# Kernel tuning notes

Measured on AMD Instinct MI355X. Metric: run time of the kernel, lower is better.

## Reference

```python
import jax, jax.numpy as jnp
import numpy as np

# Config mirrors init_kwargs
H_FULL, W_FULL = 360, 720
SCALE = 4
H_LO, W_LO = H_FULL // SCALE, W_FULL // SCALE  # 90, 180
LMAX = H_LO                  # 90
MMAX = W_LO // 2 + 1         # 91
C = 128                      # embed_dim
NL = 4                       # num_layers
INP_CH, OUT_CH = 2, 2
MLP_HID = int(C * 2.0)
EPS = 1e-5


def rfft2_trunc(x):
    # RealFFT2.forward: ortho rfft2, keep first ceil(LMAX/2) and last floor(LMAX/2) lat modes, first MMAX lon modes
    y = jnp.fft.rfft2(x, norm="ortho")
    lt = (LMAX + 1) // 2
    lb = LMAX - lt
    return jnp.concatenate([y[..., :lt, :MMAX], y[..., y.shape[-2] - lb:, :MMAX]], axis=-2)


def irfft2_pad(y, H, W):
    # InverseRealFFT2: zero-pad truncated modes back to full spectrum, ortho irfft2
    lt = (LMAX + 1) // 2
    lb = LMAX - lt
    full = jnp.zeros(y.shape[:-2] + (H, W // 2 + 1), dtype=y.dtype)
    full = full.at[..., :lt, :MMAX].set(y[..., :lt, :])
    full = full.at[..., H - lb:, :MMAX].set(y[..., lt:, :])
    return jnp.fft.irfft2(full, s=(H, W), norm="ortho")


def inorm(x, w, b):
    # InstanceNorm2d(affine=True): per-sample, per-channel over spatial dims, biased var
    mu = x.mean(axis=(-2, -1), keepdims=True)
    var = x.var(axis=(-2, -1), keepdims=True)
    xn = (x - mu) * jax.lax.rsqrt(var + EPS)
    return xn * w[None, :, None, None] + b[None, :, None, None]


def conv1x1(x, w):  # w: [Cout, Cin], bias=False
    return jnp.einsum('bihw,oi->bohw', x, w)


def gelu(x):
    return jax.nn.gelu(x, approximate=False)


def fno_block(x, n0w, n0b, swr, swi, iw, n1w, n1b, mw1, mw2, out_hw):
    in_hw = x.shape[-2:]
    xn = inorm(x, n0w, n0b)
    # SpectralConv (dhconv): complex per-l channel mixing in truncated spectral space
    Xc = rfft2_trunc(xn)                                   # [B,C,LMAX,MMAX] complex
    scale_res = tuple(in_hw) != tuple(out_hw)
    residual = irfft2_pad(Xc, out_hw[0], out_hw[1]) if scale_res else xn
    w = swr + 1j * swi                                      # [Cin,Cout,LMAX]
    Yc = jnp.einsum('bilm,iol->bolm', Xc, w)
    h = irfft2_pad(Yc, out_hw[0], out_hw[1])
    h = h + conv1x1(residual, iw)                           # inner linear skip
    h = gelu(h)                                             # act_layer0
    h = inorm(h, n1w, n1b)                                  # norm1
    h = conv1x1(gelu(conv1x1(h, mw1)), mw2)                 # MLP (1x1 convs)
    return h + residual                                     # outer identity skip


def setup_inputs() -> dict:
    key = jax.random.key(0)
    ks = jax.random.split(key, 16)
    s = 1.0 / np.sqrt(C)
    inp = {
        "x": jax.random.normal(ks[0], (1, INP_CH, H_FULL, W_FULL), jnp.float32),
        # encoder: inp_chans -> C -> C (encoder_ratio=1)
        "enc_w1": jax.random.normal(ks[1], (C, INP_CH), jnp.float32) * (1.0 / np.sqrt(INP_CH)),
        "enc_w2": jax.random.normal(ks[2], (C, C), jnp.float32) * s,
        # per-layer stacked block params
        "n0w": jnp.ones((NL, C), jnp.float32),
        "n0b": jnp.zeros((NL, C), jnp.float32),
        "swr": jax.random.normal(ks[3], (NL, C, C, LMAX), jnp.float32) * (1.0 / C),
        "swi": jax.random.normal(ks[4], (NL, C, C, LMAX), jnp.float32) * (1.0 / C),
        "iw": jax.random.normal(ks[5], (NL, C, C), jnp.float32) * s,
        "n1w": jnp.ones((NL, C), jnp.float32),
        "n1b": jnp.zeros((NL, C), jnp.float32),
        "mw1": jax.random.normal(ks[6], (NL, MLP_HID, C), jnp.float32) * s,
        "mw2": jax.random.normal(ks[7], (NL, C, MLP_HID), jnp.float32) * (1.0 / np.sqrt(MLP_HID)),
        # decoder: (C + inp_chans) -> C -> out_chans (big_skip concat)
        "dec_w1": jax.random.normal(ks[8], (C, C + INP_CH), jnp.float32) * (1.0 / np.sqrt(C + INP_CH)),
        "dec_w2": jax.random.normal(ks[9], (OUT_CH, C), jnp.float32) * s,
    }
    return inp


def reference(x, enc_w1, enc_w2, n0w, n0b, swr, swi, iw, n1w, n1b, mw1, mw2, dec_w1, dec_w2):
    big_res = x
    h = conv1x1(gelu(conv1x1(x, enc_w1)), enc_w2)           # encoder
    out_shapes = [(H_LO, W_LO)] * (NL - 1) + [(H_FULL, W_FULL)]
    for l in range(NL):
        h = fno_block(h, n0w[l], n0b[l], swr[l], swi[l], iw[l],
                      n1w[l], n1b[l], mw1[l], mw2[l], out_shapes[l])
    h = jnp.concatenate([h, big_res], axis=1)               # big skip
    h = conv1x1(gelu(conv1x1(h, dec_w1)), dec_w2)           # decoder
    return h
```

## Files before the change

kernel.cpp:

```cpp
#include <hip/hip_runtime.h>
#include <hip/hip_bf16.h>
#include <math.h>

typedef __attribute__((ext_vector_type(8))) short short8v;
typedef __attribute__((ext_vector_type(4))) float f32x4;
typedef unsigned short u16;

__device__ __forceinline__ float gelu_f(float x) {
    return 0.5f * x * (1.0f + erff(x * 0.70710678118654752f));
}
__device__ __forceinline__ float bf2f(u16 u) {
    union { unsigned int i; float f; } v; v.i = ((unsigned int)u) << 16; return v.f;
}
__device__ __forceinline__ u16 f2bf(float f) {
    union { float f; unsigned int i; } v; v.f = f;
    unsigned int r = v.i + 0x7FFFu + ((v.i >> 16) & 1u);
    return (u16)(r >> 16);
}
__device__ __forceinline__ short8v negbf(short8v a) {
    uint4 u = *(uint4*)&a;
    u.x ^= 0x80008000u; u.y ^= 0x80008000u; u.z ^= 0x80008000u; u.w ^= 0x80008000u;
    return *(short8v*)&u;
}

__device__ __forceinline__ uint4 load8(const u16* p) { return *(const uint4*)p; }
__device__ __forceinline__ uint4 load8(const float* p) {
    float4 a = *(const float4*)p;
    float4 b = *(const float4*)(p + 4);
    union { uint4 u; u16 e[8]; } r;
    r.e[0] = f2bf(a.x); r.e[1] = f2bf(a.y); r.e[2] = f2bf(a.z); r.e[3] = f2bf(a.w);
    r.e[4] = f2bf(b.x); r.e[5] = f2bf(b.y); r.e[6] = f2bf(b.z); r.e[7] = f2bf(b.w);
    return r.u;
}
__device__ __forceinline__ float rdD(const u16* p) { return bf2f(*p); }
__device__ __forceinline__ float rdD(const float* p) { return *p; }
__device__ __forceinline__ void stO(u16* p, float v) { *p = f2bf(v); }
__device__ __forceinline__ void stO(float* p, float v) { *p = v; }

template<int BMODE, class TA, class TB, class TD, class TO>
__global__ __launch_bounds__(256) void gemm_t(
    const TA* __restrict__ A1, const TB* __restrict__ B1,
    const TA* __restrict__ A2, const TB* __restrict__ B2,
    const TD* __restrict__ D, TO* __restrict__ O,
    int M, int N, int Kp, int neg2, int act,
    long long sAb, long long sAm,
    long long sBb, long long sBr,
    long long sDb, long long sDm,
    long long sOb, long long sOm)
{
    __shared__ __align__(16) u16 As[64 * 32];
    __shared__ __align__(16) u16 Bs[BMODE ? 32 * 68 : 64 * 32];
    const int tid = threadIdx.x;
    const long long b = blockIdx.z;
    const int bm0 = blockIdx.y * 64;
    const int bn0 = blockIdx.x * 64;
    const int lane = tid & 63;
    const int wave = tid >> 6;
    const int wr = (wave >> 1) * 32;
    const int wc = (wave & 1) * 32;
    const int fr = lane & 15;
    const int fg = lane >> 4;
    const int arow = tid >> 2, achk = tid & 3;

    f32x4 acc[2][2];
#pragma unroll
    for (int i = 0; i < 2; ++i)
#pragma unroll
        for (int j = 0; j < 2; ++j) acc[i][j] = (f32x4){0.f, 0.f, 0.f, 0.f};

    const int nph = A2 ? 2 : 1;
    for (int ph = 0; ph < nph; ++ph) {
        const TA* Ap = (ph ? A2 : A1) + b * sAb;
        const TB* Bp = (ph ? B2 : B1) + b * sBb;
        const unsigned int sgn = (ph && neg2) ? 0x80008000u : 0u;
        for (int k0 = 0; k0 < Kp; k0 += 32) {
            uint4 av = load8(Ap + (long long)(bm0 + arow) * sAm + k0 + achk * 8);
            av.x ^= sgn; av.y ^= sgn; av.z ^= sgn; av.w ^= sgn;
            uint4 bv;
            if (BMODE == 0) {
                bv = load8(Bp + (long long)(bn0 + arow) * sBr + k0 + achk * 8);
            } else {
                const int bk = tid >> 3, bnc = tid & 7;
                bv = load8(Bp + (long long)(k0 + bk) * sBr + bn0 + bnc * 8);
            }
            __syncthreads();
            *(uint4*)(&As[arow * 32 + ((achk ^ ((arow >> 1) & 3)) * 8)]) = av;
            if (BMODE == 0) {
                *(uint4*)(&Bs[arow * 32 + ((achk ^ ((arow >> 1) & 3)) * 8)]) = bv;
            } else {
                const int bk = tid >> 3, bnc = tid & 7;
                *(uint2*)(&Bs[bk * 68 + bnc * 8]) = make_uint2(bv.x, bv.y);
                *(uint2*)(&Bs[bk * 68 + bnc * 8 + 4]) = make_uint2(bv.z, bv.w);
            }
            __syncthreads();
            short8v afrag[2], bfrag[2];
#pragma unroll
            for (int i = 0; i < 2; ++i) {
                int r = wr + i * 16 + fr;
                afrag[i] = *(const short8v*)(&As[r * 32 + ((fg ^ ((r >> 1) & 3)) * 8)]);
            }
            if (BMODE == 0) {
#pragma unroll
                for (int j = 0; j < 2; ++j) {
                    int r = wc + j * 16 + fr;
                    bfrag[j] = *(const short8v*)(&Bs[r * 32 + ((fg ^ ((r >> 1) & 3)) * 8)]);
                }
            } else {
#pragma unroll
                for (int j = 0; j < 2; ++j) {
                    int col = wc + j * 16 + fr;
                    short8v v;
#pragma unroll
                    for (int e = 0; e < 8; ++e) v[e] = (short)Bs[(fg * 8 + e) * 68 + col];
                    bfrag[j] = v;
                }
            }
#pragma unroll
            for (int i = 0; i < 2; ++i)
#pragma unroll
                for (int j = 0; j < 2; ++j)
                    acc[i][j] = __builtin_amdgcn_mfma_f32_16x16x32_bf16(afrag[i], bfrag[j], acc[i][j], 0, 0, 0);
        }
    }
#pragma unroll
    for (int i = 0; i < 2; ++i) {
#pragma unroll
        for (int j = 0; j < 2; ++j) {
            int col = bn0 + wc + j * 16 + fr;
            if (col >= N) continue;
#pragma unroll
            for (int r = 0; r < 4; ++r) {
                int row = bm0 + wr + i * 16 + fg * 4 + r;
                if (row >= M) continue;
                float v = acc[i][j][r];
                if (D) v += rdD(D + b * sDb + (long long)row * sDm + col);
                if (act) v = gelu_f(v);
                stO(O + b * sOb + (long long)row * sOm + col, v);
            }
        }
    }
}

template<class TA, class TB, class TD, class TO>
__global__ __launch_bounds__(256) void gemm_ts(
    const TA* __restrict__ A, const TB* __restrict__ B,
    const TD* __restrict__ D, TO* __restrict__ O,
    int M, int N, int Kp, int act,
    long long sAm, long long sBr,
    long long sDm, long long sOm)
{
    __shared__ __align__(16) u16 As[64 * 32];
    __shared__ __align__(16) u16 Bs[64 * 32];
    const int tid = threadIdx.x;
    int lid = blockIdx.x + (int)gridDim.x * blockIdx.y;
    int total = (int)(gridDim.x * gridDim.y);
    int nx, ny;
    if ((lid & ~15) + 16 <= total) {
        nx = (lid >> 3) & 1;
        ny = ((lid >> 4) << 3) + (lid & 7);
    } else {
        nx = lid & 1;
        ny = lid >> 1;
    }
    const int bm0 = ny * 64;
    const int bn0 = nx * 64;
    const int lane = tid & 63;
    const int wave = tid >> 6;
    const int wr = (wave >> 1) * 32;
    const int wc = (wave & 1) * 32;
    const int fr = lane & 15;
    const int fg = lane >> 4;
    const int arow = tid >> 2, achk = tid & 3;
    const int aswz = (achk ^ ((arow >> 1) & 3)) * 8;

    f32x4 acc[2][2];
#pragma unroll
    for (int i = 0; i < 2; ++i)
#pragma unroll
        for (int j = 0; j < 2; ++j) acc[i][j] = (f32x4){0.f, 0.f, 0.f, 0.f};

    for (int k0 = 0; k0 < Kp; k0 += 32) {
        uint4 av = load8(A + (long long)(bm0 + arow) * sAm + k0 + achk * 8);
        uint4 bv = load8(B + (long long)(bn0 + arow) * sBr + k0 + achk * 8);
        __syncthreads();
        *(uint4*)(&As[arow * 32 + aswz]) = av;
        *(uint4*)(&Bs[arow * 32 + aswz]) = bv;
        __syncthreads();
        short8v afrag[2], bfrag[2];
#pragma unroll
        for (int i = 0; i < 2; ++i) {
            int r = wr + i * 16 + fr;
            afrag[i] = *(const short8v*)(&As[r * 32 + ((fg ^ ((r >> 1) & 3)) * 8)]);
        }
#pragma unroll
        for (int j = 0; j < 2; ++j) {
            int r = wc + j * 16 + fr;
            bfrag[j] = *(const short8v*)(&Bs[r * 32 + ((fg ^ ((r >> 1) & 3)) * 8)]);
        }
#pragma unroll
        for (int i = 0; i < 2; ++i)
#pragma unroll
            for (int j = 0; j < 2; ++j)
                acc[i][j] = __builtin_amdgcn_mfma_f32_16x16x32_bf16(afrag[i], bfrag[j], acc[i][j], 0, 0, 0);
    }
#pragma unroll
    for (int i = 0; i < 2; ++i) {
#pragma unroll
        for (int j = 0; j < 2; ++j) {
            int col = bn0 + wc + j * 16 + fr;
            if (col >= N) continue;
#pragma unroll
            for (int r = 0; r < 4; ++r) {
                int row = bm0 + wr + i * 16 + fg * 4 + r;
                if (row >= M) continue;
                float v = acc[i][j][r];
                if (D) v += rdD(D + (long long)row * sDm + col);
                if (act) v = gelu_f(v);
                stO(O + (long long)row * sOm + col, v);
            }
        }
    }
}

template<int BMODE, int MODE, class TA, class TB, class TO>
__global__ __launch_bounds__(256) void gemm_t2(
    const TA* __restrict__ A1, const TA* __restrict__ A2,
    const TB* __restrict__ B1, const TB* __restrict__ B2,
    TO* __restrict__ O1, TO* __restrict__ O2,
    int M, int N, int Kp, int s2neg,
    long long sAb, long long sAm,
    long long sBb, long long sBr,
    long long sOb, long long sOm)
{
    __shared__ __align__(16) u16 As1[64 * 32], As2[64 * 32];
    __shared__ __align__(16) u16 Bs1[BMODE ? 32 * 68 : 64 * 32];
    __shared__ __align__(16) u16 Bs2[(MODE == 1) ? 16 : (BMODE ? 32 * 68 : 64 * 32)];
    const int tid = threadIdx.x;
    const long long b = blockIdx.z;
    const int bm0 = blockIdx.y * 64;
    const int bn0 = blockIdx.x * 64;
    const int lane = tid & 63;
    const int wave = tid >> 6;
    const int wr = (wave >> 1) * 32;
    const int wc = (wave & 1) * 32;
    const int fr = lane & 15;
    const int fg = lane >> 4;
    const int arow = tid >> 2, achk = tid & 3;
    const int aswz = (achk ^ ((arow >> 1) & 3)) * 8;

    f32x4 acc1[2][2], acc2[2][2];
#pragma unroll
    for (int i = 0; i < 2; ++i)
#pragma unroll
        for (int j = 0; j < 2; ++j) {
            acc1[i][j] = (f32x4){0.f, 0.f, 0.f, 0.f};
            acc2[i][j] = (f32x4){0.f, 0.f, 0.f, 0.f};
        }

    const TA* A1b = A1 + b * sAb;
    const TA* A2b = A2 + b * sAb;
    const TB* B1b = B1 + b * sBb;
    const TB* B2b = (MODE == 0) ? B2 + b * sBb : B1;

    for (int k0 = 0; k0 < Kp; k0 += 32) {
        long long aoff = (long long)(bm0 + arow) * sAm + k0 + achk * 8;
        uint4 av1 = load8(A1b + aoff);
        uint4 av2 = load8(A2b + aoff);
        uint4 bv1, bv2;
        if (BMODE == 0) {
            long long boff = (long long)(bn0 + arow) * sBr + k0 + achk * 8;
            bv1 = load8(B1b + boff);
            if (MODE == 0) bv2 = load8(B2b + boff);
        } else {
            const int bk = tid >> 3, bnc = tid & 7;
            long long boff = (long long)(k0 + bk) * sBr + bn0 + bnc * 8;
            bv1 = load8(B1b + boff);
            if (MODE == 0) bv2 = load8(B2b + boff);
        }
        __syncthreads();
        *(uint4*)(&As1[arow * 32 + aswz]) = av1;
        *(uint4*)(&As2[arow * 32 + aswz]) = av2;
        if (BMODE == 0) {
            *(uint4*)(&Bs1[arow * 32 + aswz]) = bv1;
            if (MODE == 0) *(uint4*)(&Bs2[arow * 32 + aswz]) = bv2;
        } else {
            const int bk = tid >> 3, bnc = tid & 7;
            *(uint2*)(&Bs1[bk * 68 + bnc * 8]) = make_uint2(bv1.x, bv1.y);
            *(uint2*)(&Bs1[bk * 68 + bnc * 8 + 4]) = make_uint2(bv1.z, bv1.w);
            if (MODE == 0) {
                *(uint2*)(&Bs2[bk * 68 + bnc * 8]) = make_uint2(bv2.x, bv2.y);
                *(uint2*)(&Bs2[bk * 68 + bnc * 8 + 4]) = make_uint2(bv2.z, bv2.w);
            }
        }
        __syncthreads();
        short8v a1f[2], a2f[2], b1f[2], b2f[2];
#pragma unroll
        for (int i = 0; i < 2; ++i) {
            int r = wr + i * 16 + fr;
            int o = r * 32 + ((fg ^ ((r >> 1) & 3)) * 8);
            a1f[i] = *(const short8v*)(&As1[o]);
            a2f[i] = *(const short8v*)(&As2[o]);
        }
        if (BMODE == 0) {
#pragma unroll
            for (int j = 0; j < 2; ++j) {
                int r = wc + j * 16 + fr;
                int o = r * 32 + ((fg ^ ((r >> 1) & 3)) * 8);
                b1f[j] = *(const short8v*)(&Bs1[o]);
                if (MODE == 0) b2f[j] = *(const short8v*)(&Bs2[o]);
            }
        } else {
#pragma unroll
            for (int j = 0; j < 2; ++j) {
                int col = wc + j * 16 + fr;
                short8v v1, v2;
#pragma unroll
                for (int e = 0; e < 8; ++e) {
                    v1[e] = (short)Bs1[(fg * 8 + e) * 68 + col];
                    if (MODE == 0) v2[e] = (short)Bs2[(fg * 8 + e) * 68 + col];
                }
                b1f[j] = v1;
                if (MODE == 0) b2f[j] = v2;
            }
        }
        if (MODE == 1) {
#pragma unroll
            for (int i = 0; i < 2; ++i)
#pragma unroll
                for (int j = 0; j < 2; ++j) {
                    acc1[i][j] = __builtin_amdgcn_mfma_f32_16x16x32_bf16(a1f[i], b1f[j], acc1[i][j], 0, 0, 0);
                    acc2[i][j] = __builtin_amdgcn_mfma_f32_16x16x32_bf16(a2f[i], b1f[j], acc2[i][j], 0, 0, 0);
                }
        } else {
            short8v a2p[2], a2m[2];
#pragma unroll
            for (int i = 0; i < 2; ++i) {
                a2p[i] = s2neg ? negbf(a2f[i]) : a2f[i];
                a2m[i] = s2neg ? a2f[i] : negbf(a2f[i]);
            }
#pragma unroll
            for (int i = 0; i < 2; ++i)
#pragma unroll
                for (int j = 0; j < 2; ++j) {
                    acc1[i][j] = __builtin_amdgcn_mfma_f32_16x16x32_bf16(a1f[i], b1f[j], acc1[i][j], 0, 0, 0);
                    acc1[i][j] = __builtin_amdgcn_mfma_f32_16x16x32_bf16(a2p[i], b2f[j], acc1[i][j], 0, 0, 0);
                    acc2[i][j] = __builtin_amdgcn_mfma_f32_16x16x32_bf16(a1f[i], b2f[j], acc2[i][j], 0, 0, 0);
                    acc2[i][j] = __builtin_amdgcn_mfma_f32_16x16x32_bf16(a2m[i], b1f[j], acc2[i][j], 0, 0, 0);
                }
        }
    }
#pragma unroll
    for (int i = 0; i < 2; ++i) {
#pragma unroll
        for (int j = 0; j < 2; ++j) {
            int col = bn0 + wc + j * 16 + fr;
            if (col >= N) continue;
#pragma unroll
            for (int r = 0; r < 4; ++r) {
                int row = bm0 + wr + i * 16 + fg * 4 + r;
                if (row >= M) continue;
                long long oi = b * sOb + (long long)row * sOm + col;
                stO(O1 + oi, acc1[i][j][r]);
                stO(O2 + oi, acc2[i][j][r]);
            }
        }
    }
}

__global__ void gen_fwdW_T(u16* Cm, u16* Sm, int RP, int KP, int W, int MM) {
    int idx = blockIdx.x * blockDim.x + threadIdx.x;
    if (idx >= RP * KP) return;
    int m = idx / KP, w = idx % KP;
    float cv = 0.f, sv = 0.f;
    if (m < MM && w < W) {
        int t = (m * w) % W;
        float arg = 2.0f * (float)t / (float)W;
        float s = 1.0f / sqrtf((float)W);
        cv = cospif(arg) * s; sv = -sinpif(arg) * s;
    }
    Cm[idx] = f2bf(cv); Sm[idx] = f2bf(sv);
}
__global__ void gen_fwdH(u16* Cm, u16* Sm, int RP, int KP, int H) {
    int idx = blockIdx.x * blockDim.x + threadIdx.x;
    if (idx >= RP * KP) return;
    int l = idx / KP, h = idx % KP;
    float cv = 0.f, sv = 0.f;
    if (l < 90 && h < H) {
        int ll = (l < 45) ? l : l + H - 90;
        int t = (ll * h) % H;
        float arg = 2.0f * (float)t / (float)H;
        float s = 1.0f / sqrtf((float)H);
        cv = cospif(arg) * s; sv = sinpif(arg) * s;
    }
    Cm[idx] = f2bf(cv); Sm[idx] = f2bf(sv);
}
__global__ void gen_invH(u16* Cm, u16* Sm, int RP, int KP, int H) {
    int idx = blockIdx.x * blockDim.x + threadIdx.x;
    if (idx >= RP * KP) return;
    int y = idx / KP, l = idx % KP;
    float cv = 0.f, sv = 0.f;
    if (y < H && l < 90) {
        int ll = (l < 45) ? l : l + H - 90;
        int t = (ll * y) % H;
        float arg = 2.0f * (float)t / (float)H;
        float s = 1.0f / sqrtf((float)H);
        cv = cospif(arg) * s; sv = sinpif(arg) * s;
    }
    Cm[idx] = f2bf(cv); Sm[idx] = f2bf(sv);
}
__global__ void gen_invW_T(u16* Cm, u16* Sm, int RP, int KP, int W, int MM) {
    int idx = blockIdx.x * blockDim.x + threadIdx.x;
    if (idx >= RP * KP) return;
    int w = idx / KP, m = idx % KP;
    float cv = 0.f, sv = 0.f;
    if (w < W && m < MM) {
        int t = (m * w) % W;
        float arg = 2.0f * (float)t / (float)W;
        bool nyq = (2 * m == W);
        float wt = (m == 0 || nyq) ? 1.0f : 2.0f;
        float s = wt / sqrtf((float)W);
        cv = cospif(arg) * s;
        sv = nyq ? 0.f : sinpif(arg) * s;
    }
    Cm[idx] = f2bf(cv); Sm[idx] = f2bf(sv);
}

__global__ void w2bf(const float* __restrict__ in, u16* __restrict__ out, int R, int K, int rs) {
    int idx = blockIdx.x * blockDim.x + threadIdx.x;
    if (idx >= R * K) return;
    int r = idx / K, c = idx % K;
    out[idx] = f2bf(in[(long long)r * rs + c]);
}
__global__ void transp_sw(const float* __restrict__ in, u16* __restrict__ out) {
    __shared__ float t[32][33];
    int l0 = blockIdx.x * 32, ci0 = blockIdx.y * 32, co = blockIdx.z;
    int tx = threadIdx.x, ty = threadIdx.y;
#pragma unroll
    for (int rr = 0; rr < 4; ++rr) {
        int ci = ci0 + ty + rr * 8;
        int l = l0 + tx;
        t[ty + rr * 8][tx] = (l < 90) ? in[((long long)ci * 128 + co) * 90 + l] : 0.f;
    }
    __syncthreads();
#pragma unroll
    for (int rr = 0; rr < 4; ++rr) {
        int l = l0 + ty + rr * 8;
        int ci = ci0 + tx;
        if (l < 90) out[((long long)l * 128 + co) * 128 + ci] = f2bf(t[tx][ty + rr * 8]);
    }
}

__global__ __launch_bounds__(256) void stats_cl_bf(const u16* __restrict__ x, long long P,
                                                   float2* __restrict__ part, int nch) {
    int chunk = blockIdx.x;
    int c = threadIdx.x & 127;
    int h = threadIdx.x >> 7;
    long long beg = P * chunk / nch, end = P * (chunk + 1) / nch;
    float s = 0.f, q = 0.f;
    long long p = beg + h;
    for (; p + 14 < end; p += 16) {
        float v[8];
#pragma unroll
        for (int u = 0; u < 8; ++u) v[u] = bf2f(x[(p + 2 * u) * 128 + c]);
#pragma unroll
        for (int u = 0; u < 8; ++u) { s += v[u]; q += v[u] * v[u]; }
    }
    for (; p < end; p += 2) {
        float v = bf2f(x[p * 128 + c]);
        s += v; q += v * v;
    }
    __shared__ float rs[256], rq[256];
    rs[threadIdx.x] = s; rq[threadIdx.x] = q;
    __syncthreads();
    if (threadIdx.x < 128)
        part[(long long)c * nch + chunk] = make_float2(rs[c] + rs[c + 128], rq[c] + rq[c + 128]);
}
__global__ __launch_bounds__(256) void stats_cl_f32(const float* __restrict__ x, long long P,
                                                    float2* __restrict__ part, int nch) {
    int chunk = blockIdx.x;
    long long beg = P * chunk / nch, end = P * (chunk + 1) / nch;
    int c32 = threadIdx.x & 31;
    int pr  = threadIdx.x >> 5;
    float s[4], q[4];
#pragma unroll
    for (int k = 0; k < 4; ++k) { s[k] = 0.f; q[k] = 0.f; }
    for (long long p = beg + pr; p < end; p += 8) {
        float4 v = *(const float4*)(x + p * 128 + c32 * 4);
        float e[4] = {v.x, v.y, v.z, v.w};
#pragma unroll
        for (int k = 0; k < 4; ++k) { s[k] += e[k]; q[k] += e[k] * e[k]; }
    }
#pragma unroll
    for (int k = 0; k < 4; ++k) {
        s[k] += __shfl_xor(s[k], 32); q[k] += __shfl_xor(q[k], 32);
    }
    __shared__ float2 lds[4][128];
    int wv = threadIdx.x >> 6, lane = threadIdx.x & 63;
    if (lane < 32) {
#pragma unroll
        for (int k = 0; k < 4; ++k) lds[wv][lane * 4 + k] = make_float2(s[k], q[k]);
    }
    __syncthreads();
    if (threadIdx.x < 128) {
        float2 a = lds[0][threadIdx.x], b2 = lds[1][threadIdx.x];
        float2 c2 = lds[2][threadIdx.x], d2 = lds[3][threadIdx.x];
        part[(long long)threadIdx.x * nch + chunk] =
            make_float2(a.x + b2.x + c2.x + d2.x, a.y + b2.y + c2.y + d2.y);
    }
}
__global__ void stats_fin(const float2* __restrict__ part, int nch, float Pf,
                          const float* __restrict__ w, const float* __restrict__ b,
                          float2* __restrict__ st) {
    int c = threadIdx.x;
    float s = 0.f, q = 0.f;
    for (int i = 0; i < nch; ++i) { float2 p = part[(long long)c * nch + i]; s += p.x; q += p.y; }
    float mu = s / Pf;
    float var = q / Pf - mu * mu;
    float inv = rsqrtf(var + 1e-5f);
    float sc = w[c] * inv;
    st[c] = make_float2(sc, b[c] - mu * sc);
}
__global__ __launch_bounds__(256) void norm_apply_bf(const u16* __restrict__ src, u16* __restrict__ dst,
                                                     long long n8, const float2* __restrict__ st) {
    long long i = (long long)blockIdx.x * 256 + threadIdx.x;
    if (i >= n8) return;
    int c0 = (int)((i * 8) & 127);
    uint4 v = *(const uint4*)(src + i * 8);
    union { uint4 u; u16 e[8]; } in, out;
    in.u = v;
#pragma unroll
    for (int k = 0; k < 8; ++k) {
        float2 s = st[c0 + k];
        out.e[k] = f2bf(bf2f(in.e[k]) * s.x + s.y);
    }
    *(uint4*)(dst + i * 8) = out.u;
}
__global__ __launch_bounds__(256) void norm_apply_f32(const float4* __restrict__ src, float4* __restrict__ dst,
                                                      long long n4, const float2* __restrict__ st) {
    long long i = (long long)blockIdx.x * 256 + threadIdx.x;
    if (i >= n4) return;
    int c0 = (int)((i * 4) & 127);
    float4 v = src[i];
    float2 s0 = st[c0], s1 = st[c0 + 1], s2 = st[c0 + 2], s3 = st[c0 + 3];
    v.x = v.x * s0.x + s0.y;
    v.y = v.y * s1.x + s1.y;
    v.z = v.z * s2.x + s2.y;
    v.w = v.w * s3.x + s3.y;
    dst[i] = v;
}

__global__ __launch_bounds__(256) void enc_front(const float* __restrict__ x, const float* __restrict__ w1,
                                                 u16* __restrict__ out, long long P) {
    long long idx = (long long)blockIdx.x * 256 + threadIdx.x;
    if (idx >= P * 16) return;
    long long p = idx >> 4;
    int c0 = (int)(idx & 15) * 8;
    float x0 = x[p], x1 = x[P + p];
    union { uint4 u; u16 e[8]; } o;
#pragma unroll
    for (int k = 0; k < 8; ++k) {
        int c = c0 + k;
        o.e[k] = f2bf(gelu_f(w1[c * 2] * x0 + w1[c * 2 + 1] * x1));
    }
    *(uint4*)(out + p * 128 + c0) = o.u;
}
__global__ __launch_bounds__(256) void dec_mid(u16* __restrict__ s, const float* __restrict__ dw1,
                                               const float* __restrict__ x, long long P) {
    long long idx = (long long)blockIdx.x * 256 + threadIdx.x;
    if (idx >= P * 16) return;
    long long p = idx >> 4;
    int c0 = (int)(idx & 15) * 8;
    float x0 = x[p], x1 = x[P + p];
    union { uint4 u; u16 e[8]; } io;
    io.u = *(const uint4*)(s + p * 128 + c0);
#pragma unroll
    for (int k = 0; k < 8; ++k) {
        int c = c0 + k;
        io.e[k] = f2bf(gelu_f(bf2f(io.e[k]) + dw1[c * 130 + 128] * x0 + dw1[c * 130 + 129] * x1));
    }
    *(uint4*)(s + p * 128 + c0) = io.u;
}
__global__ __launch_bounds__(256) void dec_back(const u16* __restrict__ d1, const float* __restrict__ w2,
                                                float* __restrict__ out, long long P) {
    __shared__ float w2s[256];
    w2s[threadIdx.x] = w2[threadIdx.x];
    __syncthreads();
    int lane = threadIdx.x & 63;
    long long pix = (long long)blockIdx.x * 4 + (threadIdx.x >> 6);
    unsigned int pr = *(const unsigned int*)(d1 + pix * 128 + lane * 2);
    float b0 = bf2f((u16)(pr & 0xFFFF)), b1 = bf2f((u16)(pr >> 16));
    float s0 = b0 * w2s[lane * 2] + b1 * w2s[lane * 2 + 1];
    float s1 = b0 * w2s[128 + lane * 2] + b1 * w2s[128 + lane * 2 + 1];
#pragma unroll
    for (int off = 1; off < 64; off <<= 1) {
        s0 += __shfl_xor(s0, off);
        s1 += __shfl_xor(s1, off);
    }
    if (lane == 0) { out[pix] = s0; out[P + pix] = s1; }
}

__global__ void zero_out(float* p, long long n) {
    long long i = (long long)blockIdx.x * 256 + threadIdx.x;
    if (i < n) p[i] = 0.f;
}

extern "C" void kernel_launch(void* const* d_in, const int* in_sizes, int n_in,
                              void* d_out, int out_size, void* d_ws, size_t ws_size,
                              hipStream_t stream)
{
    const int HF = 360, WF = 720, HL = 90, WL = 180, C = 128, MM = 91;
    const long long PF = (long long)HF * WF;
    const long long PL = (long long)HL * WL;
    (void)in_sizes; (void)n_in;

    const float* x      = (const float*)d_in[0];
    const float* enc_w1 = (const float*)d_in[1];
    const float* enc_w2 = (const float*)d_in[2];
    const float* n0w    = (const float*)d_in[3];
    const float* n0b    = (const float*)d_in[4];
    const float* swr    = (const float*)d_in[5];
    const float* swi    = (const float*)d_in[6];
    const float* iw     = (const float*)d_in[7];
    const float* n1w    = (const float*)d_in[8];
    const float* n1b    = (const float*)d_in[9];
    const float* mw1    = (const float*)d_in[10];
    const float* mw2    = (const float*)d_in[11];
    const float* dec_w1 = (const float*)d_in[12];
    const float* dec_w2 = (const float*)d_in[13];
    float* outp = (float*)d_out;

    u16* ws = (u16*)d_ws;
    long long off = 0;
    auto alloc = [&](long long n) { u16* p = ws + off; off += (n + 31) & ~31LL; return p; };
    auto allocF = [&](long long n) { return (float*)alloc(2 * n); };

    u16*   FULL = alloc(PF * C);
    u16*   RES  = alloc(PF * C);
    u16*   S1r  = alloc(96LL * 384 * 128);
    u16*   S1i  = alloc(96LL * 384 * 128);
    float* Xr   = allocF(96LL * 96 * 128);
    float* Xi   = allocF(96LL * 96 * 128);
    float* Yr   = allocF(96LL * 96 * 128);
    float* Yi   = allocF(96LL * 96 * 128);
    u16*   G1r  = alloc(360LL * 96 * 128);
    u16*   G1i  = alloc(360LL * 96 * 128);
    u16*   G3r  = alloc(360LL * 96 * 128);
    u16*   G3i  = alloc(360LL * 96 * 128);
    float* Rlo  = allocF(PL * C);
    float* L0   = allocF(PL * C);
    u16*   HID  = alloc(43200LL * 256);
    u16*   WtR  = alloc(90LL * 128 * 128);
    u16*   WtI  = alloc(90LL * 128 * 128);
    u16* encw2b = alloc(128 * 128);
    u16* iwb    = alloc(128 * 128);
    u16* m1b    = alloc(256 * 128);
    u16* m2b    = alloc(128 * 256);
    u16* dw1b   = alloc(128 * 128);
    u16* CwTc_h = alloc(128 * 736); u16* CwTs_h = alloc(128 * 736);
    u16* CwTc_l = alloc(128 * 192); u16* CwTs_l = alloc(128 * 192);
    u16* Chc_h  = alloc(128 * 384); u16* Chs_h  = alloc(128 * 384);
    u16* Chc_l  = alloc(128 * 96);  u16* Chs_l  = alloc(128 * 96);
    u16* C2c_h  = alloc(384 * 96);  u16* C2s_h  = alloc(384 * 96);
    u16* C2c_l  = alloc(128 * 96);  u16* C2s_l  = alloc(128 * 96);
    u16* CwIc_h = alloc(768 * 96);  u16* CwIs_h = alloc(768 * 96);
    u16* CwIc_l = alloc(192 * 96);  u16* CwIs_l = alloc(192 * 96);
    float2* PART = (float2*)alloc(128 * 256 * 4);
    float2* STb  = (float2*)alloc(128 * 4);
    alloc(64 * 1024);

    if ((size_t)(off * 2) > ws_size) {
        zero_out<<<(int)((out_size + 255) / 256), 256, 0, stream>>>(outp, out_size);
        return;
    }

    auto grid3 = [](int M, int N, int batch) {
        return dim3((unsigned)((N + 63) / 64), (unsigned)((M + 63) / 64), (unsigned)batch);
    };
    auto inormB = [&](const u16* src, u16* dst, long long P, int nch,
                      const float* w, const float* b) {
        stats_cl_bf<<<nch, 256, 0, stream>>>(src, P, PART, nch);
        stats_fin<<<1, 128, 0, stream>>>(PART, nch, (float)P, w, b, STb);
        long long n8 = P * 128 / 8;
        norm_apply_bf<<<(int)((n8 + 255) / 256), 256, 0, stream>>>(src, dst, n8, STb);
    };
    auto inormF = [&](const float* src, float* dst, long long P, int nch,
                      const float* w, const float* b) {
        stats_cl_f32<<<nch, 256, 0, stream>>>(src, P, PART, nch);
        stats_fin<<<1, 128, 0, stream>>>(PART, nch, (float)P, w, b, STb);
        long long n4 = P * 128 / 4;
        norm_apply_f32<<<(int)((n4 + 255) / 256), 256, 0, stream>>>(
            (const float4*)src, (float4*)dst, n4, STb);
    };

    const u16* nullU = nullptr;
    const float* nullF = nullptr;

    {
        int n;
        n = 128 * 736; gen_fwdW_T<<<(n + 255) / 256, 256, 0, stream>>>(CwTc_h, CwTs_h, 128, 736, 720, MM);
        n = 128 * 192; gen_fwdW_T<<<(n + 255) / 256, 256, 0, stream>>>(CwTc_l, CwTs_l, 128, 192, 180, MM);
        n = 128 * 384; gen_fwdH<<<(n + 255) / 256, 256, 0, stream>>>(Chc_h, Chs_h, 128, 384, 360);
        n = 128 * 96;  gen_fwdH<<<(n + 255) / 256, 256, 0, stream>>>(Chc_l, Chs_l, 128, 96, 90);
        n = 384 * 96;  gen_invH<<<(n + 255) / 256, 256, 0, stream>>>(C2c_h, C2s_h, 384, 96, 360);
        n = 128 * 96;  gen_invH<<<(n + 255) / 256, 256, 0, stream>>>(C2c_l, C2s_l, 128, 96, 90);
        n = 768 * 96;  gen_invW_T<<<(n + 255) / 256, 256, 0, stream>>>(CwIc_h, CwIs_h, 768, 96, 720, MM);
        n = 192 * 96;  gen_invW_T<<<(n + 255) / 256, 256, 0, stream>>>(CwIc_l, CwIs_l, 192, 96, 180, MM);
        n = 128 * 128; w2bf<<<(n + 255) / 256, 256, 0, stream>>>(enc_w2, encw2b, 128, 128, 128);
        n = 128 * 128; w2bf<<<(n + 255) / 256, 256, 0, stream>>>(dec_w1, dw1b, 128, 128, 130);
    }

    enc_front<<<(int)((PF * 16 + 255) / 256), 256, 0, stream>>>(x, enc_w1, RES, PF);
    gemm_ts<u16, u16, u16, u16><<<grid3((int)PF, 128, 1), 256, 0, stream>>>(
        RES, encw2b, nullU, FULL, (int)PF, 128, 128, 0, 128, 128, 0, 128);

    const long long s96 = 96LL * 128;

    for (int l = 0; l < 4; ++l) {
        const bool inHi = (l == 0), outHi = (l == 3);
        const int Hin = inHi ? HF : HL, Win = inHi ? WF : WL;
        const int Hout = outHi ? HF : HL, Wout = outHi ? WF : WL;
        const long long Pout = (long long)Hout * Wout;
        const int hdim = inHi ? 384 : 96;
        const int Wp = inHi ? 736 : 192;
        const int hp = inHi ? 384 : 96;
        const u16* CwTc = inHi ? CwTc_h : CwTc_l;  const u16* CwTs = inHi ? CwTs_h : CwTs_l;
        const u16* Chc  = inHi ? Chc_h  : Chc_l;   const u16* Chs  = inHi ? Chs_h  : Chs_l;
        const u16* C2c  = outHi ? C2c_h : C2c_l;   const u16* C2s  = outHi ? C2s_h : C2s_l;
        const u16* CwIc = outHi ? CwIc_h : CwIc_l; const u16* CwIs = outHi ? CwIs_h : CwIs_l;

        {
            dim3 gt(3, 4, 128); dim3 bt(32, 8);
            transp_sw<<<gt, bt, 0, stream>>>(swr + (long long)l * C * C * 90, WtR);
            transp_sw<<<gt, bt, 0, stream>>>(swi + (long long)l * C * C * 90, WtI);
            int n = 128 * 128; w2bf<<<(n + 255) / 256, 256, 0, stream>>>(iw + (long long)l * C * C, iwb, 128, 128, 128);
            n = 256 * 128; w2bf<<<(n + 255) / 256, 256, 0, stream>>>(mw1 + (long long)l * 256 * C, m1b, 256, 128, 128);
            n = 128 * 256; w2bf<<<(n + 255) / 256, 256, 0, stream>>>(mw2 + (long long)l * C * 256, m2b, 128, 256, 256);
        }

        if (inHi) {
            inormB(FULL, RES, PF, 256, n0w + l * C, n0b + l * C);
            gemm_t2<1, 1, u16, u16, u16><<<grid3(96, 128, Hin), 256, 0, stream>>>(
                CwTc, CwTs, RES, nullU, S1r, S1i, 96, 128, Wp, 0,
                0, Wp, (long long)Win * 128, 128, 128, (long long)hdim * 128);
        } else {
            inormF(Rlo, L0, PL, 128, n0w + l * C, n0b + l * C);
            gemm_t2<1, 1, u16, float, u16><<<grid3(96, 128, Hin), 256, 0, stream>>>(
                CwTc, CwTs, L0, nullF, S1r, S1i, 96, 128, Wp, 0,
                0, Wp, (long long)Win * 128, 128, 128, (long long)hdim * 128);
        }

        gemm_t2<1, 0, u16, u16, float><<<grid3(96, 128, 96), 256, 0, stream>>>(
            Chc, Chs, S1r, S1i, Xr, Xi, 96, 128, hp, 0,
            0, hp, (long long)hdim * 128, 128, 128, s96);

        if (inHi || outHi) {
            gemm_t2<1, 0, u16, float, u16><<<grid3(Hout, 128, 96), 256, 0, stream>>>(
                C2c, C2s, Xr, Xi, G3r, G3i, Hout, 128, 96, 1,
                0, 96, 128, s96, 128, s96);
        }

        gemm_t2<0, 0, float, u16, float><<<grid3(96, 128, 90), 256, 0, stream>>>(
            Xr, Xi, WtR, WtI, Yr, Yi, 96, 128, 128, 1,
            s96, 128, 128LL * 128, 128, 128, s96);

        gemm_t2<1, 0, u16, float, u16><<<grid3(Hout, 128, 96), 256, 0, stream>>>(
            C2c, C2s, Yr, Yi, G1r, G1i, Hout, 128, 96, 1,
            0, 96, s96, 128, 128, s96);

        if (!outHi) {
            gemm_t<1, u16, u16, u16, float><<<grid3(Wout, 128, Hout), 256, 0, stream>>>(
                CwIc, G1r, CwIs, G1i, nullU, Rlo, Wout, 128, 96, 1, 0,
                0, 96, s96, 128, 0, 0, (long long)Wout * 128, 128);
            if (inHi)
                gemm_t<1, u16, u16, u16, float><<<grid3(Wout, 128, Hout), 256, 0, stream>>>(
                    CwIc, G3r, CwIs, G3i, nullU, L0, Wout, 128, 96, 1, 0,
                    0, 96, s96, 128, 0, 0, (long long)Wout * 128, 128);
            gemm_t<0, float, u16, float, float><<<grid3((int)Pout, 128, 1), 256, 0, stream>>>(
                L0, iwb, nullF, nullU, Rlo, Rlo, (int)Pout, 128, 128, 0, 1,
                0, 128, 0, 128, 0, 128, 0, 128);
            inormF(Rlo, Rlo, Pout, 128, n1w + l * C, n1b + l * C);
            gemm_t<0, float, u16, u16, u16><<<grid3((int)Pout, 256, 1), 256, 0, stream>>>(
                Rlo, m1b, nullF, nullU, nullU, HID, (int)Pout, 256, 128, 0, 1,
                0, 128, 0, 128, 0, 0, 0, 256);
            gemm_t<0, u16, u16, float, float><<<grid3((int)Pout, 128, 1), 256, 0, stream>>>(
                HID, m2b, nullU, nullU, L0, Rlo, (int)Pout, 128, 256, 0, 0,
                0, 256, 0, 256, 0, 128, 0, 128);
        } else {
            gemm_t<1, u16, u16, u16, u16><<<grid3(Wout, 128, Hout), 256, 0, stream>>>(
                CwIc, G1r, CwIs, G1i, nullU, FULL, Wout, 128, 96, 1, 0,
                0, 96, s96, 128, 0, 0, (long long)Wout * 128, 128);
            gemm_t<1, u16, u16, u16, u16><<<grid3(Wout, 128, Hout), 256, 0, stream>>>(
                CwIc, G3r, CwIs, G3i, nullU, RES, Wout, 128, 96, 1, 0,
                0, 96, s96, 128, 0, 0, (long long)Wout * 128, 128);
            gemm_ts<u16, u16, u16, u16><<<grid3((int)Pout, 128, 1), 256, 0, stream>>>(
                RES, iwb, FULL, FULL, (int)Pout, 128, 128, 1, 128, 128, 128, 128);
            inormB(FULL, FULL, Pout, 256, n1w + l * C, n1b + l * C);
            const int nchunk = 6;
            const long long chM = Pout / nchunk;
            for (int ch = 0; ch < nchunk; ++ch) {
                long long o2 = ch * chM * 128;
                gemm_t<0, u16, u16, u16, u16><<<grid3((int)chM, 256, 1), 256, 0, stream>>>(
                    FULL + o2, m1b, nullU, nullU, nullU, HID, (int)chM, 256, 128, 0, 1,
                    0, 128, 0, 128, 0, 0, 0, 256);
                gemm_ts<u16, u16, u16, u16><<<grid3((int)chM, 128, 1), 256, 0, stream>>>(
                    HID, m2b, RES + o2, FULL + o2, (int)chM, 128, 256, 0, 256, 256, 128, 128);
            }
        }
    }

    gemm_ts<u16, u16, u16, u16><<<grid3((int)PF, 128, 1), 256, 0, stream>>>(
        FULL, dw1b, nullU, RES, (int)PF, 128, 128, 0, 128, 128, 0, 128);
    dec_mid<<<(int)((PF * 16 + 255) / 256), 256, 0, stream>>>(RES, dec_w1, x, PF);
    dec_back<<<(int)(PF / 4), 256, 0, stream>>>(RES, dec_w2, outp, PF);
}
```

Before: 1.285 ms.

## Fuse MLP two GEMMs into one kernel with LDS hidden tile; fuse decoder tail

Adds a gemm_mlp kernel that computes the hidden layer for a 64-row tile, applies GELU, keeps the 64x256 bf16 hidden tile in shared memory, then runs the second GEMM with the residual add. This removes the HID global round-trip and the chunked launch loop for the full-resolution layer. Separately, dec_mid and dec_back are merged so the decoder's skip term and GELU are applied on the fly, avoiding one pass over the full-resolution buffer. The price is that weights are read straight from global memory rather than staged in LDS, the kernel uses about 48KB of LDS (which may lower occupancy), and the A-tile load has no row bound check.

```diff
diff --git a/kernel.cpp b/kernel.cpp
--- a/kernel.cpp
+++ b/kernel.cpp
@@ -217,6 +217,117 @@
                 if (D) v += rdD(D + (long long)row * sDm + col);
                 if (act) v = gelu_f(v);
                 stO(O + (long long)row * sOm + col, v);
+            }
+        }
+    }
+}
+
+template<class TA, class TD, class TO>
+__global__ __launch_bounds__(256) void gemm_mlp(
+    const TA* __restrict__ A, const u16* __restrict__ W1, const u16* __restrict__ W2,
+    const TD* __restrict__ D, TO* __restrict__ O,
+    int M, long long sAm, long long sDm, long long sOm)
+{
+    __shared__ __align__(16) u16 As4[4][64 * 32];
+    __shared__ __align__(16) u16 Hs[8][64 * 32];
+    const int tid = threadIdx.x;
+    const int bm0 = blockIdx.x * 64;
+    const int lane = tid & 63;
+    const int wave = tid >> 6;
+    const int wr = (wave >> 1) * 32;
+    const int wc = (wave & 1) * 32;
+    const int fr = lane & 15;
+    const int fg = lane >> 4;
+    const int arow = tid >> 2, achk = tid & 3;
+    const int aswz = (achk ^ ((arow >> 1) & 3)) * 8;
+
+#pragma unroll
+    for (int kt = 0; kt < 4; ++kt) {
+        uint4 av = load8(A + (long long)(bm0 + arow) * sAm + kt * 32 + achk * 8);
+        *(uint4*)(&As4[kt][arow * 32 + aswz]) = av;
+    }
+    __syncthreads();
+
+#pragma unroll
+    for (int nb = 0; nb < 4; ++nb) {
+        f32x4 acc[2][2];
+#pragma unroll
+        for (int i = 0; i < 2; ++i)
+#pragma unroll
+            for (int j = 0; j < 2; ++j) acc[i][j] = (f32x4){0.f, 0.f, 0.f, 0.f};
+#pragma unroll
+        for (int kt = 0; kt < 4; ++kt) {
+            short8v af[2], bf[2];
+#pragma unroll
+            for (int i = 0; i < 2; ++i) {
+                int r = wr + i * 16 + fr;
+                af[i] = *(const short8v*)(&As4[kt][r * 32 + ((fg ^ ((r >> 1) & 3)) * 8)]);
+            }
+#pragma unroll
+            for (int j = 0; j < 2; ++j) {
+                int col = wc + nb * 64 + j * 16 + fr;
+                bf[j] = *(const short8v*)(W1 + (long long)col * 128 + kt * 32 + fg * 8);
+            }
+#pragma unroll
+            for (int i = 0; i < 2; ++i)
+#pragma unroll
+                for (int j = 0; j < 2; ++j)
+                    acc[i][j] = __builtin_amdgcn_mfma_f32_16x16x32_bf16(af[i], bf[j], acc[i][j], 0, 0, 0);
+        }
+#pragma unroll
+        for (int i = 0; i < 2; ++i)
+#pragma unroll
+            for (int j = 0; j < 2; ++j) {
+                int col = wc + nb * 64 + j * 16 + fr;
+                int kt2 = col >> 5, kc = (col >> 3) & 3, ke = col & 7;
+#pragma unroll
+                for (int r = 0; r < 4; ++r) {
+                    int row = wr + i * 16 + fg * 4 + r;
+                    Hs[kt2][row * 32 + ((kc ^ ((row >> 1) & 3)) * 8) + ke] = f2bf(gelu_f(acc[i][j][r]));
+                }
+            }
+    }
+    __syncthreads();
+
+#pragma unroll
+    for (int nb2 = 0; nb2 < 2; ++nb2) {
+        f32x4 acc2[2][2];
+#pragma unroll
+        for (int i = 0; i < 2; ++i)
+#pragma unroll
+            for (int j = 0; j < 2; ++j) acc2[i][j] = (f32x4){0.f, 0.f, 0.f, 0.f};
+#pragma unroll
+        for (int kt = 0; kt < 8; ++kt) {
+            short8v af[2], bf[2];
+#pragma unroll
+            for (int i = 0; i < 2; ++i) {
+                int r = wr + i * 16 + fr;
+                af[i] = *(const short8v*)(&Hs[kt][r * 32 + ((fg ^ ((r >> 1) & 3)) * 8)]);
+            }
+#pragma unroll
+            for (int j = 0; j < 2; ++j) {
+                int col = nb2 * 64 + wc + j * 16 + fr;
+                bf[j] = *(const short8v*)(W2 + (long long)col * 256 + kt * 32 + fg * 8);
+            }
+#pragma unroll
+            for (int i = 0; i < 2; ++i)
+#pragma unroll
+                for (int j = 0; j < 2; ++j)
+                    acc2[i][j] = __builtin_amdgcn_mfma_f32_16x16x32_bf16(af[i], bf[j], acc2[i][j], 0, 0, 0);
+        }
+#pragma unroll
+        for (int i = 0; i < 2; ++i) {
+#pragma unroll
+            for (int j = 0; j < 2; ++j) {
+                int col = nb2 * 64 + wc + j * 16 + fr;
+#pragma unroll
+                for (int r = 0; r < 4; ++r) {
+                    int row = bm0 + wr + i * 16 + fg * 4 + r;
+                    if (row >= M) continue;
+                    float v = acc2[i][j][r];
+                    if (D) v += rdD(D + (long long)row * sDm + col);
+                    stO(O + (long long)row * sOm + col, v);
+                }
             }
         }
     }
@@ -564,31 +675,23 @@
     }
     *(uint4*)(out + p * 128 + c0) = o.u;
 }
-__global__ __launch_bounds__(256) void dec_mid(u16* __restrict__ s, const float* __restrict__ dw1,
-                                               const float* __restrict__ x, long long P) {
-    long long idx = (long long)blockIdx.x * 256 + threadIdx.x;
-    if (idx >= P * 16) return;
-    long long p = idx >> 4;
-    int c0 = (int)(idx & 15) * 8;
-    float x0 = x[p], x1 = x[P + p];
-    union { uint4 u; u16 e[8]; } io;
-    io.u = *(const uint4*)(s + p * 128 + c0);
-#pragma unroll
-    for (int k = 0; k < 8; ++k) {
-        int c = c0 + k;
-        io.e[k] = f2bf(gelu_f(bf2f(io.e[k]) + dw1[c * 130 + 128] * x0 + dw1[c * 130 + 129] * x1));
-    }
-    *(uint4*)(s + p * 128 + c0) = io.u;
-}
-__global__ __launch_bounds__(256) void dec_back(const u16* __restrict__ d1, const float* __restrict__ w2,
+__global__ __launch_bounds__(256) void dec_fuse(const u16* __restrict__ d1, const float* __restrict__ dw1,
+                                                const float* __restrict__ x, const float* __restrict__ w2,
                                                 float* __restrict__ out, long long P) {
     __shared__ float w2s[256];
+    __shared__ float dxs[256];
     w2s[threadIdx.x] = w2[threadIdx.x];
+    {
+        int c = threadIdx.x >> 1, h = threadIdx.x & 1;
+        dxs[threadIdx.x] = dw1[c * 130 + 128 + h];
+    }
     __syncthreads();
     int lane = threadIdx.x & 63;
     long long pix = (long long)blockIdx.x * 4 + (threadIdx.x >> 6);
+    float x0 = x[pix], x1 = x[P + pix];
     unsigned int pr = *(const unsigned int*)(d1 + pix * 128 + lane * 2);
-    float b0 = bf2f((u16)(pr & 0xFFFF)), b1 = bf2f((u16)(pr >> 16));
+    float b0 = bf2f(f2bf(gelu_f(bf2f((u16)(pr & 0xFFFF)) + dxs[4 * lane]     * x0 + dxs[4 * lane + 1] * x1)));
+    float b1 = bf2f(f2bf(gelu_f(bf2f((u16)(pr >> 16))    + dxs[4 * lane + 2] * x0 + dxs[4 * lane + 3] * x1)));
     float s0 = b0 * w2s[lane * 2] + b1 * w2s[lane * 2 + 1];
     float s1 = b0 * w2s[128 + lane * 2] + b1 * w2s[128 + lane * 2 + 1];
 #pragma unroll
@@ -648,7 +751,6 @@
     u16*   G3i  = alloc(360LL * 96 * 128);
     float* Rlo  = allocF(PL * C);
     float* L0   = allocF(PL * C);
-    u16*   HID  = alloc(43200LL * 256);
     u16*   WtR  = alloc(90LL * 128 * 128);
     u16*   WtI  = alloc(90LL * 128 * 128);
     u16* encw2b = alloc(128 * 128);
@@ -779,12 +881,8 @@
                 L0, iwb, nullF, nullU, Rlo, Rlo, (int)Pout, 128, 128, 0, 1,
                 0, 128, 0, 128, 0, 128, 0, 128);
             inormF(Rlo, Rlo, Pout, 128, n1w + l * C, n1b + l * C);
-            gemm_t<0, float, u16, u16, u16><<<grid3((int)Pout, 256, 1), 256, 0, stream>>>(
-                Rlo, m1b, nullF, nullU, nullU, HID, (int)Pout, 256, 128, 0, 1,
-                0, 128, 0, 128, 0, 0, 0, 256);
-            gemm_t<0, u16, u16, float, float><<<grid3((int)Pout, 128, 1), 256, 0, stream>>>(
-                HID, m2b, nullU, nullU, L0, Rlo, (int)Pout, 128, 256, 0, 0,
-                0, 256, 0, 256, 0, 128, 0, 128);
+            gemm_mlp<float, float, float><<<dim3((unsigned)((Pout + 63) / 64)), 256, 0, stream>>>(
+                Rlo, m1b, m2b, L0, Rlo, (int)Pout, 128, 128, 128);
         } else {
             gemm_t<1, u16, u16, u16, u16><<<grid3(Wout, 128, Hout), 256, 0, stream>>>(
                 CwIc, G1r, CwIs, G1i, nullU, FULL, Wout, 128, 96, 1, 0,
@@ -795,21 +893,12 @@
             gemm_ts<u16, u16, u16, u16><<<grid3((int)Pout, 128, 1), 256, 0, stream>>>(
                 RES, iwb, FULL, FULL, (int)Pout, 128, 128, 1, 128, 128, 128, 128);
             inormB(FULL, FULL, Pout, 256, n1w + l * C, n1b + l * C);
-            const int nchunk = 6;
-            const long long chM = Pout / nchunk;
-            for (int ch = 0; ch < nchunk; ++ch) {
-                long long o2 = ch * chM * 128;
-                gemm_t<0, u16, u16, u16, u16><<<grid3((int)chM, 256, 1), 256, 0, stream>>>(
-                    FULL + o2, m1b, nullU, nullU, nullU, HID, (int)chM, 256, 128, 0, 1,
-                    0, 128, 0, 128, 0, 0, 0, 256);
-                gemm_ts<u16, u16, u16, u16><<<grid3((int)chM, 128, 1), 256, 0, stream>>>(
-                    HID, m2b, RES + o2, FULL + o2, (int)chM, 128, 256, 0, 256, 256, 128, 128);
-            }
+            gemm_mlp<u16, u16, u16><<<dim3((unsigned)((Pout + 63) / 64)), 256, 0, stream>>>(
+                FULL, m1b, m2b, RES, FULL, (int)Pout, 128, 128, 128);
         }
     }
 
     gemm_ts<u16, u16, u16, u16><<<grid3((int)PF, 128, 1), 256, 0, stream>>>(
         FULL, dw1b, nullU, RES, (int)PF, 128, 128, 0, 128, 128, 0, 128);
-    dec_mid<<<(int)((PF * 16 + 255) / 256), 256, 0, stream>>>(RES, dec_w1, x, PF);
-    dec_back<<<(int)(PF / 4), 256, 0, stream>>>(RES, dec_w2, outp, PF);
-}
+    dec_fuse<<<(int)(PF / 4), 256, 0, stream>>>(RES, dec_w1, x, dec_w2, outp, PF);
+}
```

Result: faster. 1.242 ms (median of 3 runs) (-3.4%).

## Fuse MLP GEMMs through LDS and merge decoder mid/back kernels

Applied to the files above, without the earlier changes.

Adds a gemm_mlp kernel that computes the first MLP GEMM with GELU for a 64-row tile, stages the bf16 hidden activations in per-wave LDS, and feeds them straight into the second GEMM plus residual add. This removes the HID intermediate buffer's global write and read and the chunked two-kernel launch loop, for both the low-res and full-res layers. Weight fragments are read directly from global/L2 by every wave instead of being tiled through shared memory, which may add L2 traffic. The decoder's bias/GELU step is folded into the final 2-channel projection kernel, saving one full-resolution pass over the activation tensor.

```diff
diff --git a/kernel.cpp b/kernel.cpp
--- a/kernel.cpp
+++ b/kernel.cpp
@@ -218,6 +218,68 @@
                 if (act) v = gelu_f(v);
                 stO(O + (long long)row * sOm + col, v);
             }
+        }
+    }
+}
+
+template<class TA, class TD, class TO>
+__global__ __launch_bounds__(256) void gemm_mlp(
+    const TA* __restrict__ A, const u16* __restrict__ W1, const u16* __restrict__ W2,
+    const TD* __restrict__ D, TO* __restrict__ O,
+    int M, long long sAm, long long sDm, long long sOm)
+{
+    __shared__ __align__(16) unsigned int Hw[4][16 * 132];
+    const int tid = threadIdx.x;
+    const int bm0 = blockIdx.x * 64;
+    const int lane = tid & 63;
+    const int wave = tid >> 6;
+    const int p = lane & 15;
+    const int g = lane >> 4;
+    const int R0 = bm0 + wave * 16;
+
+    short8v xfrag[4];
+#pragma unroll
+    for (int kt = 0; kt < 4; ++kt) {
+        uint4 v = load8(A + (long long)(R0 + p) * sAm + kt * 32 + g * 8);
+        xfrag[kt] = *(short8v*)&v;
+    }
+
+    unsigned int* Hrow = &Hw[wave][p * 132];
+
+#pragma unroll
+    for (int h = 0; h < 16; ++h) {
+        f32x4 acc = (f32x4){0.f, 0.f, 0.f, 0.f};
+#pragma unroll
+        for (int kt = 0; kt < 4; ++kt) {
+            short8v wf = *(const short8v*)(W1 + (long long)(h * 16 + p) * 128 + kt * 32 + g * 8);
+            acc = __builtin_amdgcn_mfma_f32_16x16x32_bf16(wf, xfrag[kt], acc, 0, 0, 0);
+        }
+        unsigned int lo = (unsigned int)f2bf(gelu_f(acc[0])) | ((unsigned int)f2bf(gelu_f(acc[1])) << 16);
+        unsigned int hi = (unsigned int)f2bf(gelu_f(acc[2])) | ((unsigned int)f2bf(gelu_f(acc[3])) << 16);
+        *(uint2*)(Hrow + 8 * h + 2 * g) = make_uint2(lo, hi);
+    }
+
+    short8v hfrag[8];
+#pragma unroll
+    for (int c = 0; c < 8; ++c)
+        hfrag[c] = *(const short8v*)(Hrow + 16 * c + 4 * g);
+
+#pragma unroll
+    for (int o = 0; o < 8; ++o) {
+        f32x4 acc = (f32x4){0.f, 0.f, 0.f, 0.f};
+#pragma unroll
+        for (int c = 0; c < 8; ++c) {
+            short8v wf = *(const short8v*)(W2 + (long long)(o * 16 + p) * 256 + c * 32 + g * 8);
+            acc = __builtin_amdgcn_mfma_f32_16x16x32_bf16(hfrag[c], wf, acc, 0, 0, 0);
+        }
+        int col = o * 16 + p;
+#pragma unroll
+        for (int r = 0; r < 4; ++r) {
+            int row = R0 + g * 4 + r;
+            if (row >= M) continue;
+            float v = acc[r];
+            if (D) v += rdD(D + (long long)row * sDm + col);
+            stO(O + (long long)row * sOm + col, v);
         }
     }
 }
@@ -564,31 +626,23 @@
     }
     *(uint4*)(out + p * 128 + c0) = o.u;
 }
-__global__ __launch_bounds__(256) void dec_mid(u16* __restrict__ s, const float* __restrict__ dw1,
-                                               const float* __restrict__ x, long long P) {
-    long long idx = (long long)blockIdx.x * 256 + threadIdx.x;
-    if (idx >= P * 16) return;
-    long long p = idx >> 4;
-    int c0 = (int)(idx & 15) * 8;
-    float x0 = x[p], x1 = x[P + p];
-    union { uint4 u; u16 e[8]; } io;
-    io.u = *(const uint4*)(s + p * 128 + c0);
-#pragma unroll
-    for (int k = 0; k < 8; ++k) {
-        int c = c0 + k;
-        io.e[k] = f2bf(gelu_f(bf2f(io.e[k]) + dw1[c * 130 + 128] * x0 + dw1[c * 130 + 129] * x1));
-    }
-    *(uint4*)(s + p * 128 + c0) = io.u;
-}
-__global__ __launch_bounds__(256) void dec_back(const u16* __restrict__ d1, const float* __restrict__ w2,
+__global__ __launch_bounds__(256) void dec_fuse(const u16* __restrict__ d1, const float* __restrict__ dw1,
+                                                const float* __restrict__ x, const float* __restrict__ w2,
                                                 float* __restrict__ out, long long P) {
     __shared__ float w2s[256];
+    __shared__ float dxsT[256];
     w2s[threadIdx.x] = w2[threadIdx.x];
+    {
+        int k = threadIdx.x >> 6, ln = threadIdx.x & 63;
+        dxsT[threadIdx.x] = dw1[(2 * ln + (k >> 1)) * 130 + 128 + (k & 1)];
+    }
     __syncthreads();
     int lane = threadIdx.x & 63;
     long long pix = (long long)blockIdx.x * 4 + (threadIdx.x >> 6);
+    float x0 = x[pix], x1 = x[P + pix];
     unsigned int pr = *(const unsigned int*)(d1 + pix * 128 + lane * 2);
-    float b0 = bf2f((u16)(pr & 0xFFFF)), b1 = bf2f((u16)(pr >> 16));
+    float b0 = bf2f(f2bf(gelu_f(bf2f((u16)(pr & 0xFFFF)) + dxsT[lane]       * x0 + dxsT[64 + lane]  * x1)));
+    float b1 = bf2f(f2bf(gelu_f(bf2f((u16)(pr >> 16))    + dxsT[128 + lane] * x0 + dxsT[192 + lane] * x1)));
     float s0 = b0 * w2s[lane * 2] + b1 * w2s[lane * 2 + 1];
     float s1 = b0 * w2s[128 + lane * 2] + b1 * w2s[128 + lane * 2 + 1];
 #pragma unroll
@@ -648,7 +702,6 @@
     u16*   G3i  = alloc(360LL * 96 * 128);
     float* Rlo  = allocF(PL * C);
     float* L0   = allocF(PL * C);
-    u16*   HID  = alloc(43200LL * 256);
     u16*   WtR  = alloc(90LL * 128 * 128);
     u16*   WtI  = alloc(90LL * 128 * 128);
     u16* encw2b = alloc(128 * 128);
@@ -779,12 +832,8 @@
                 L0, iwb, nullF, nullU, Rlo, Rlo, (int)Pout, 128, 128, 0, 1,
                 0, 128, 0, 128, 0, 128, 0, 128);
             inormF(Rlo, Rlo, Pout, 128, n1w + l * C, n1b + l * C);
-            gemm_t<0, float, u16, u16, u16><<<grid3((int)Pout, 256, 1), 256, 0, stream>>>(
-                Rlo, m1b, nullF, nullU, nullU, HID, (int)Pout, 256, 128, 0, 1,
-                0, 128, 0, 128, 0, 0, 0, 256);
-            gemm_t<0, u16, u16, float, float><<<grid3((int)Pout, 128, 1), 256, 0, stream>>>(
-                HID, m2b, nullU, nullU, L0, Rlo, (int)Pout, 128, 256, 0, 0,
-                0, 256, 0, 256, 0, 128, 0, 128);
+            gemm_mlp<float, float, float><<<dim3((unsigned)((Pout + 63) / 64)), 256, 0, stream>>>(
+                Rlo, m1b, m2b, L0, Rlo, (int)Pout, 128, 128, 128);
         } else {
             gemm_t<1, u16, u16, u16, u16><<<grid3(Wout, 128, Hout), 256, 0, stream>>>(
                 CwIc, G1r, CwIs, G1i, nullU, FULL, Wout, 128, 96, 1, 0,
@@ -795,21 +844,12 @@
             gemm_ts<u16, u16, u16, u16><<<grid3((int)Pout, 128, 1), 256, 0, stream>>>(
                 RES, iwb, FULL, FULL, (int)Pout, 128, 128, 1, 128, 128, 128, 128);
             inormB(FULL, FULL, Pout, 256, n1w + l * C, n1b + l * C);
-            const int nchunk = 6;
-            const long long chM = Pout / nchunk;
-            for (int ch = 0; ch < nchunk; ++ch) {
-                long long o2 = ch * chM * 128;
-                gemm_t<0, u16, u16, u16, u16><<<grid3((int)chM, 256, 1), 256, 0, stream>>>(
-                    FULL + o2, m1b, nullU, nullU, nullU, HID, (int)chM, 256, 128, 0, 1,
-                    0, 128, 0, 128, 0, 0, 0, 256);
-                gemm_ts<u16, u16, u16, u16><<<grid3((int)chM, 128, 1), 256, 0, stream>>>(
-                    HID, m2b, RES + o2, FULL + o2, (int)chM, 128, 256, 0, 256, 256, 128, 128);
-            }
+            gemm_mlp<u16, u16, u16><<<dim3((unsigned)((Pout + 63) / 64)), 256, 0, stream>>>(
+                FULL, m1b, m2b, RES, FULL, (int)Pout, 128, 128, 128);
         }
     }
 
     gemm_ts<u16, u16, u16, u16><<<grid3((int)PF, 128, 1), 256, 0, stream>>>(
         FULL, dw1b, nullU, RES, (int)PF, 128, 128, 0, 128, 128, 0, 128);
-    dec_mid<<<(int)((PF * 16 + 255) / 256), 256, 0, stream>>>(RES, dec_w1, x, PF);
-    dec_back<<<(int)(PF / 4), 256, 0, stream>>>(RES, dec_w2, outp, PF);
-}
+    dec_fuse<<<(int)(PF / 4), 256, 0, stream>>>(RES, dec_w1, x, dec_w2, outp, PF);
+}
```

Result: no change. 1.296 ms (+0.9%).
